# Kernel optimization log

Measured on AMD Instinct MI355X. Metric: run time of the kernel, lower is better.

## Reference

```python
import jax, jax.numpy as jnp
import numpy as np

B = 32; D = 512; NH = 8; DH = 64; DEPTH = 8; MLP = 2048
NC = 256; Hs = 16; Ws = 16; SHIFT = 1
INNER = NH * DH


def setup_inputs() -> dict:
    key = jax.random.key(0)
    ks = jax.random.split(key, 8)
    s = D ** -0.5
    return {
        "z": jax.random.normal(ks[0], (B, D, Hs, Ws), jnp.float32),
        "slots": jax.random.normal(ks[1], (B, NC, D), jnp.float32),
        "pos_emb": jax.random.normal(ks[2], (1, Hs * Ws, D), jnp.float32) * s,
        "slot_pos_emb": jax.random.normal(ks[3], (1, NC, D), jnp.float32) * s,
        "norm_w": jnp.ones((D,), jnp.float32),
        "norm_b": jnp.zeros((D,), jnp.float32),
        "ln1_w": jnp.ones((DEPTH, D), jnp.float32),
        "ln1_b": jnp.zeros((DEPTH, D), jnp.float32),
        "qkv_w": jax.random.normal(ks[4], (DEPTH, D, 3 * INNER), jnp.float32) * 0.02,
        "out_w": jax.random.normal(ks[5], (DEPTH, INNER, D), jnp.float32) * 0.02,
        "out_b": jnp.zeros((DEPTH, D), jnp.float32),
        "ln2_w": jnp.ones((DEPTH, D), jnp.float32),
        "ln2_b": jnp.zeros((DEPTH, D), jnp.float32),
        "mlp_w1": jax.random.normal(ks[6], (DEPTH, D, MLP), jnp.float32) * 0.02,
        "mlp_b1": jnp.zeros((DEPTH, MLP), jnp.float32),
        "mlp_w2": jax.random.normal(ks[7], (DEPTH, MLP, D), jnp.float32) * 0.02,
        "mlp_b2": jnp.zeros((DEPTH, D), jnp.float32),
    }


def _ln(x, w, b):
    m = x.mean(-1, keepdims=True)
    v = ((x - m) ** 2).mean(-1, keepdims=True)
    return (x - m) * jax.lax.rsqrt(v + 1e-5) * w + b


def reference(z, slots, pos_emb, slot_pos_emb, norm_w, norm_b,
              ln1_w, ln1_b, qkv_w, out_w, out_b,
              ln2_w, ln2_b, mlp_w1, mlp_b1, mlp_w2, mlp_b2):
    S = NC + Hs * Ws  # 512 tokens: carriers then patches
    mem = slots + slot_pos_emb                                   # [B, NC, D]
    h = z.reshape(B, D, Hs * Ws).transpose(0, 2, 1) + pos_emb    # [B, HW, D]
    x = jnp.concatenate([mem, h], axis=1)                        # [B, S, D]
    x = _ln(x, norm_w, norm_b)
    causal = jnp.tril(jnp.ones((S, S), dtype=bool))              # allowed positions
    scale = DH ** -0.5
    for i in range(DEPTH):
        y = _ln(x, ln1_w[i], ln1_b[i])
        qkv = y @ qkv_w[i]                                       # [B, S, 3*INNER]
        q, k, v = jnp.split(qkv, 3, axis=-1)
        q = q.reshape(B, S, NH, DH).transpose(0, 2, 1, 3)
        k = k.reshape(B, S, NH, DH).transpose(0, 2, 1, 3)
        v = v.reshape(B, S, NH, DH).transpose(0, 2, 1, 3)
        att = jnp.einsum('bhqd,bhkd->bhqk', q, k) * scale
        att = jnp.where(causal, att, jnp.float32(-1e30))
        att = jax.nn.softmax(att, axis=-1)
        o = jnp.einsum('bhqk,bhkd->bhqd', att, v)
        o = o.transpose(0, 2, 1, 3).reshape(B, S, INNER)
        x = x + o @ out_w[i] + out_b[i]
        y = _ln(x, ln2_w[i], ln2_b[i])
        x = x + jax.nn.gelu(y @ mlp_w1[i] + mlp_b1[i], approximate=False) @ mlp_w2[i] + mlp_b2[i]
    out = x[:, NC - SHIFT:NC - SHIFT + Hs * Ws]                  # shifted slice
    return out.transpose(0, 2, 1).reshape(B, D, Hs, Ws)
```

## Files before the change

kernel.cpp:

```cpp
#include <hip/hip_runtime.h>
#include <hip/hip_bf16.h>
#include <math.h>

#define Bb 32
#define Dd 512
#define Ss 512
#define NHh 8
#define DHh 64
#define MLPm 2048
#define NCc 256
#define INNERi 512
#define Mrows (Bb*Ss)

typedef __bf16 bf16x8 __attribute__((ext_vector_type(8)));
typedef float floatx4 __attribute__((ext_vector_type(4)));

__device__ __forceinline__ void load_lds16(const void* g, void* l) {
  __builtin_amdgcn_global_load_lds(
      (__attribute__((address_space(1))) void*)(g),
      (__attribute__((address_space(3))) void*)(l), 16, 0, 0);
}

__device__ __forceinline__ int swz(int row, int seg) {
  return row * 64 + (((seg) ^ (row & 7)) << 3);
}

__global__ void transpose_w(const float* __restrict__ in, __hip_bfloat16* __restrict__ out,
                            int K, int N, size_t in_ls, size_t out_ls)
{
  __shared__ float tile[32][33];
  in  += (size_t)blockIdx.z * in_ls;
  out += (size_t)blockIdx.z * out_ls;
  int n0 = blockIdx.x * 32, k0 = blockIdx.y * 32;
  int tx = threadIdx.x;
  #pragma unroll
  for (int i = threadIdx.y; i < 32; i += 8)
    tile[i][tx] = in[(size_t)(k0 + i) * N + n0 + tx];
  __syncthreads();
  #pragma unroll
  for (int i = threadIdx.y; i < 32; i += 8)
    out[(size_t)(n0 + i) * K + k0 + tx] = __float2bfloat16(tile[tx][i]);
}

__global__ void prologue_kernel(const float* __restrict__ z, const float* __restrict__ slots,
                                const float* __restrict__ pos, const float* __restrict__ spos,
                                const float* __restrict__ nw, const float* __restrict__ nb,
                                float* __restrict__ x)
{
  int row = blockIdx.x;
  int b = row >> 9, s = row & 511;
  int lane = threadIdx.x;
  float v[8];
  float sum = 0.f;
  #pragma unroll
  for (int j = 0; j < 8; ++j) {
    int d = lane + j * 64;
    float t;
    if (s < NCc) t = slots[((size_t)b * NCc + s) * Dd + d] + spos[(size_t)s * Dd + d];
    else {
      int sp = s - NCc;
      t = z[((size_t)b * Dd + d) * 256 + sp] + pos[(size_t)sp * Dd + d];
    }
    v[j] = t; sum += t;
  }
  #pragma unroll
  for (int o = 32; o; o >>= 1) sum += __shfl_xor(sum, o);
  float mean = sum * (1.f / Dd);
  float vs = 0.f;
  #pragma unroll
  for (int j = 0; j < 8; ++j) { float d = v[j] - mean; vs += d * d; }
  #pragma unroll
  for (int o = 32; o; o >>= 1) vs += __shfl_xor(vs, o);
  float rs = rsqrtf(vs * (1.f / Dd) + 1e-5f);
  #pragma unroll
  for (int j = 0; j < 8; ++j) {
    int d = lane + j * 64;
    x[(size_t)row * Dd + d] = (v[j] - mean) * rs * nw[d] + nb[d];
  }
}

__global__ void ln_kernel(const float* __restrict__ x, const float* __restrict__ w,
                          const float* __restrict__ b, __hip_bfloat16* __restrict__ y)
{
  int row = blockIdx.x * 4 + (threadIdx.x >> 6);
  int lane = threadIdx.x & 63;
  const float* xr = x + (size_t)row * Dd;
  float v[8];
  float sum = 0.f;
  #pragma unroll
  for (int j = 0; j < 8; ++j) { v[j] = xr[lane + j * 64]; sum += v[j]; }
  #pragma unroll
  for (int o = 32; o; o >>= 1) sum += __shfl_xor(sum, o);
  float mean = sum * (1.f / Dd);
  float vs = 0.f;
  #pragma unroll
  for (int j = 0; j < 8; ++j) { float d = v[j] - mean; vs += d * d; }
  #pragma unroll
  for (int o = 32; o; o >>= 1) vs += __shfl_xor(vs, o);
  float rs = rsqrtf(vs * (1.f / Dd) + 1e-5f);
  #pragma unroll
  for (int j = 0; j < 8; ++j) {
    int d = lane + j * 64;
    y[(size_t)row * Dd + d] = __float2bfloat16((v[j] - mean) * rs * w[d] + b[d]);
  }
}

template <int MODE>
__global__ __launch_bounds__(256, 2)
void gemm_bt(const __hip_bfloat16* __restrict__ A, const __hip_bfloat16* __restrict__ Bt,
             const float* __restrict__ bias, const float* __restrict__ res,
             void* __restrict__ Out, int M, int N, int K)
{
  constexpr int BM = 128, BN = 128, BK = 64;
  __shared__ __align__(16) __hip_bfloat16 As[BM * BK];
  __shared__ __align__(16) __hip_bfloat16 Bs[BN * BK];
  const int tid = threadIdx.x;
  const int lane = tid & 63;
  const int wave = tid >> 6;

  const int NBLK = N >> 7;
  const int bid = blockIdx.x;
  const int xcd = bid & 7;
  const int j = bid >> 3;
  const int nb = j % NBLK;
  const int mt = xcd + ((j / NBLK) << 3);
  const int m0 = mt << 7;
  const int n0 = nb << 7;

  const int wm = (wave & 1) * 64;
  const int wn = (wave >> 1) * 64;
  const int quad = lane >> 4;
  const int lrow = lane & 15;

  floatx4 acc[4][4];
  #pragma unroll
  for (int i = 0; i < 4; ++i)
    #pragma unroll
    for (int jj = 0; jj < 4; ++jj) {
      floatx4 z4 = {0.f, 0.f, 0.f, 0.f};
      acc[i][jj] = z4;
    }

  for (int k0 = 0; k0 < K; k0 += BK) {
    #pragma unroll
    for (int it = 0; it < 4; ++it) {
      int c = it * 256 + tid;
      int row = c >> 3, seg = (c & 7) ^ (row & 7);
      load_lds16(A + (size_t)(m0 + row) * K + k0 + seg * 8, As + c * 8);
    }
    #pragma unroll
    for (int it = 0; it < 4; ++it) {
      int c = it * 256 + tid;
      int row = c >> 3, seg = (c & 7) ^ (row & 7);
      load_lds16(Bt + (size_t)(n0 + row) * K + k0 + seg * 8, Bs + c * 8);
    }
    __syncthreads();

    #pragma unroll
    for (int k1 = 0; k1 < BK; k1 += 32) {
      const int s0 = k1 >> 3;
      bf16x8 a[4], b[4];
      #pragma unroll
      for (int i = 0; i < 4; ++i)
        a[i] = *reinterpret_cast<const bf16x8*>(&As[swz(wm + i * 16 + lrow, s0 + quad)]);
      #pragma unroll
      for (int i = 0; i < 4; ++i)
        b[i] = *reinterpret_cast<const bf16x8*>(&Bs[swz(wn + i * 16 + lrow, s0 + quad)]);
      #pragma unroll
      for (int mi = 0; mi < 4; ++mi)
        #pragma unroll
        for (int ni = 0; ni < 4; ++ni)
          acc[mi][ni] = __builtin_amdgcn_mfma_f32_16x16x32_bf16(a[mi], b[ni], acc[mi][ni], 0, 0, 0);
    }
    __syncthreads();
  }

  #pragma unroll
  for (int mi = 0; mi < 4; ++mi) {
    #pragma unroll
    for (int r = 0; r < 4; ++r) {
      int gm = m0 + wm + mi * 16 + quad * 4 + r;
      #pragma unroll
      for (int ni = 0; ni < 4; ++ni) {
        int gn = n0 + wn + ni * 16 + lrow;
        float v = acc[mi][ni][r];
        size_t oi = (size_t)gm * N + gn;
        if (MODE == 0) {
          ((__hip_bfloat16*)Out)[oi] = __float2bfloat16(v);
        } else if (MODE == 1) {
          ((float*)Out)[oi] = v + bias[gn] + res[oi];
        } else {
          float t = v + bias[gn];
          float g = 0.5f * t * (1.0f + erff(t * 0.70710678118654752f));
          ((__hip_bfloat16*)Out)[oi] = __float2bfloat16(g);
        }
      }
    }
  }
}

#define GBAR()    asm volatile("s_barrier" ::: "memory")
#define GWAIT10() asm volatile("s_waitcnt vmcnt(10)" ::: "memory")
#define GWAIT0()  asm volatile("s_waitcnt vmcnt(0)" ::: "memory")
#define LGKM0()   do { asm volatile("s_waitcnt lgkmcnt(0)" ::: "memory"); \
                       __builtin_amdgcn_sched_barrier(0); } while (0)
#define DSR0(d,a)  asm volatile("ds_read_b128 %0, %1"             : "=v"(d) : "v"(a))
#define DSR1(d,a)  asm volatile("ds_read_b128 %0, %1 offset:1024" : "=v"(d) : "v"(a))
#define DSR2(d,a)  asm volatile("ds_read_b128 %0, %1 offset:2048" : "=v"(d) : "v"(a))
#define DSR3(d,a)  asm volatile("ds_read_b128 %0, %1 offset:3072" : "=v"(d) : "v"(a))

template <int MODE>
__global__ __launch_bounds__(512, 2)
void gemm256(const __hip_bfloat16* __restrict__ A, const __hip_bfloat16* __restrict__ Bt,
             const float* __restrict__ bias, void* __restrict__ Out,
             int M, int N, int K)
{
  extern __shared__ __hip_bfloat16 lds[];
  const int tid  = threadIdx.x;
  const int lane = tid & 63;
  const int wave = tid >> 6;
  const int wm = wave >> 2, wn = wave & 3;
  const int quad = lane >> 4, lrow = lane & 15;

  const int NBN = N >> 8;
  const int nwg = gridDim.x;
  const int bid = blockIdx.x;
  const int qq = nwg >> 3, rr = nwg & 7;
  const int xcd = bid & 7, oin = bid >> 3;
  const int wg = (xcd < rr ? xcd * (qq + 1) : rr * (qq + 1) + (xcd - rr) * qq) + oin;
  const int m0 = (wg / NBN) << 8;
  const int n0 = (wg % NBN) << 8;
  const int NT = K >> 6;

  const int srow = tid >> 2;
  const int sseg = (tid & 3) ^ ((tid >> 3) & 3);
  const __hip_bfloat16* gA = A  + (size_t)(m0 + srow) * K + sseg * 8;
  const __hip_bfloat16* gB = Bt + (size_t)(n0 + srow) * K + sseg * 8;
  const size_t gstep = (size_t)128 * K;

  __hip_bfloat16* const Abase = lds;
  __hip_bfloat16* const Bbase = lds + 32768;

  auto stageA = [&](int t, int kh) {
    int ts = t < NT ? t : NT - 1;
    int kb = ts * 64 + kh * 32;
    __hip_bfloat16* d = Abase + ((((t & 1) << 1) | kh) * 8192) + tid * 8;
    load_lds16(gA + kb, d);
    load_lds16(gA + gstep + kb, d + 4096);
  };
  auto stageB = [&](int t, int kh) {
    int ts = t < NT ? t : NT - 1;
    int kb = ts * 64 + kh * 32;
    __hip_bfloat16* d = Bbase + ((((t & 1) << 1) | kh) * 8192) + tid * 8;
    load_lds16(gB + kb, d);
    load_lds16(gB + gstep + kb, d + 4096);
  };

  floatx4 acc[2][4][4];
  #pragma unroll
  for (int mh = 0; mh < 2; ++mh)
    #pragma unroll
    for (int mi = 0; mi < 4; ++mi)
      #pragma unroll
      for (int ni = 0; ni < 4; ++ni) {
        floatx4 z4 = {0.f, 0.f, 0.f, 0.f};
        acc[mh][mi][ni] = z4;
      }

  const uint32_t ldsA = (uint32_t)(size_t)(__attribute__((address_space(3))) void*)Abase;
  const uint32_t ldsB = (uint32_t)(size_t)(__attribute__((address_space(3))) void*)Bbase;
  const uint32_t rsegb = (uint32_t)((quad ^ ((lrow >> 1) & 3)) << 4);
  const uint32_t arow_b = (uint32_t)((wm * 128 + lrow) * 64) + rsegb;
  const uint32_t brow_b = (uint32_t)((wn * 64 + lrow) * 64) + rsegb;

  stageB(0, 0); stageA(0, 0); stageB(0, 1); stageA(0, 1);
  stageB(1, 0); stageA(1, 0); stageB(1, 1);
  GWAIT10();
  GBAR();

  bf16x8 af[4], bfr[4];
  for (int t = 0; t < NT; ++t) {
    const uint32_t aS = ldsA + (uint32_t)((t & 1) * 32768);
    const uint32_t bS = ldsB + (uint32_t)((t & 1) * 32768);
    const uint32_t a0 = aS + arow_b;
    const uint32_t b0 = bS + brow_b;
    const uint32_t a1 = aS + 16384 + arow_b;
    const uint32_t b1 = bS + 16384 + brow_b;

    DSR0(bfr[0], b0); DSR1(bfr[1], b0); DSR2(bfr[2], b0); DSR3(bfr[3], b0);
    DSR0(af[0], a0);  DSR1(af[1], a0);  DSR2(af[2], a0);  DSR3(af[3], a0);
    stageA(t + 1, 1);
    GBAR();
    LGKM0();
    __builtin_amdgcn_s_setprio(1);
    #pragma unroll
    for (int mi = 0; mi < 4; ++mi)
      #pragma unroll
      for (int ni = 0; ni < 4; ++ni)
        acc[0][mi][ni] = __builtin_amdgcn_mfma_f32_16x16x32_bf16(af[mi], bfr[ni], acc[0][mi][ni], 0, 0, 0);
    __builtin_amdgcn_s_setprio(0);
    GBAR();

    DSR0(af[0], a0 + 4096); DSR1(af[1], a0 + 4096);
    DSR2(af[2], a0 + 4096); DSR3(af[3], a0 + 4096);
    stageB(t + 2, 0);
    GBAR();
    LGKM0();
    __builtin_amdgcn_s_setprio(1);
    #pragma unroll
    for (int mi = 0; mi < 4; ++mi)
      #pragma unroll
      for (int ni = 0; ni < 4; ++ni)
        acc[1][mi][ni] = __builtin_amdgcn_mfma_f32_16x16x32_bf16(af[mi], bfr[ni], acc[1][mi][ni], 0, 0, 0);
    __builtin_amdgcn_s_setprio(0);
    GWAIT10();
    GBAR();

    DSR0(bfr[0], b1); DSR1(bfr[1], b1); DSR2(bfr[2], b1); DSR3(bfr[3], b1);
    DSR0(af[0], a1);  DSR1(af[1], a1);  DSR2(af[2], a1);  DSR3(af[3], a1);
    stageA(t + 2, 0);
    GBAR();
    LGKM0();
    __builtin_amdgcn_s_setprio(1);
    #pragma unroll
    for (int mi = 0; mi < 4; ++mi)
      #pragma unroll
      for (int ni = 0; ni < 4; ++ni)
        acc[0][mi][ni] = __builtin_amdgcn_mfma_f32_16x16x32_bf16(af[mi], bfr[ni], acc[0][mi][ni], 0, 0, 0);
    __builtin_amdgcn_s_setprio(0);
    GBAR();

    DSR0(af[0], a1 + 4096); DSR1(af[1], a1 + 4096);
    DSR2(af[2], a1 + 4096); DSR3(af[3], a1 + 4096);
    stageB(t + 2, 1);
    GBAR();
    LGKM0();
    __builtin_amdgcn_s_setprio(1);
    #pragma unroll
    for (int mi = 0; mi < 4; ++mi)
      #pragma unroll
      for (int ni = 0; ni < 4; ++ni)
        acc[1][mi][ni] = __builtin_amdgcn_mfma_f32_16x16x32_bf16(af[mi], bfr[ni], acc[1][mi][ni], 0, 0, 0);
    __builtin_amdgcn_s_setprio(0);
    GWAIT10();
    GBAR();
  }

  GWAIT0();

  const int cm0 = m0 + wm * 128 + quad * 4;
  const int cn0 = n0 + wn * 64 + lrow;
  #pragma unroll
  for (int mh = 0; mh < 2; ++mh)
    #pragma unroll
    for (int mi = 0; mi < 4; ++mi)
      #pragma unroll
      for (int r = 0; r < 4; ++r) {
        const int gm = cm0 + mh * 64 + mi * 16 + r;
        #pragma unroll
        for (int ni = 0; ni < 4; ++ni) {
          const int gn = cn0 + ni * 16;
          float v = acc[mh][mi][ni][r];
          size_t oi = (size_t)gm * N + gn;
          if (MODE == 0) {
            ((__hip_bfloat16*)Out)[oi] = __float2bfloat16(v);
          } else {
            float tt = v + bias[gn];
            float g = 0.5f * tt * (1.0f + erff(tt * 0.70710678118654752f));
            ((__hip_bfloat16*)Out)[oi] = __float2bfloat16(g);
          }
        }
      }
}

__global__ __launch_bounds__(256, 2)
void attn_pair(const __hip_bfloat16* __restrict__ qkv, __hip_bfloat16* __restrict__ o)
{
  const int p = blockIdx.x;
  const int h = blockIdx.y, b = blockIdx.z;
  const int t0 = p, t1 = 7 - p;

  __shared__ __align__(16) __hip_bfloat16 Qs[2][64 * 64];
  __shared__ __align__(16) __hip_bfloat16 Ks[64 * 64];
  __shared__ __align__(16) __hip_bfloat16 Vt[64 * 64];
  __shared__ __align__(16) __hip_bfloat16 Ps[4][16 * 64];

  const int tid = threadIdx.x, lane = tid & 63, wave = tid >> 6;
  const int quad = lane >> 4, col = lane & 15;
  const size_t base = ((size_t)b * Ss) * 1536 + (size_t)h * 64;

  #pragma unroll
  for (int t = 0; t < 2; ++t) {
    const int tq = t ? t1 : t0;
    #pragma unroll
    for (int it = 0; it < 2; ++it) {
      int c = it * 256 + tid;
      int row = c >> 3, seg = c & 7;
      bf16x8 q8 = *reinterpret_cast<const bf16x8*>(
          qkv + base + (size_t)(tq * 64 + row) * 1536 + seg * 8);
      *reinterpret_cast<bf16x8*>(&Qs[t][swz(row, seg)]) = q8;
    }
  }

  bf16x8 kreg[2], vreg[2];
  auto load_kv = [&](int c0) {
    #pragma unroll
    for (int it = 0; it < 2; ++it) {
      int c = it * 256 + tid;
      kreg[it] = *reinterpret_cast<const bf16x8*>(
          qkv + base + 512 + (size_t)(c0 * 64 + (c >> 3)) * 1536 + (c & 7) * 8);
    }
    #pragma unroll
    for (int it = 0; it < 2; ++it) {
      int row = tid & 63, seg = it * 4 + wave;
      vreg[it] = *reinterpret_cast<const bf16x8*>(
          qkv + base + 1024 + (size_t)(c0 * 64 + row) * 1536 + seg * 8);
    }
  };
  auto store_kv = [&]() {
    #pragma unroll
    for (int it = 0; it < 2; ++it) {
      int c = it * 256 + tid;
      *reinterpret_cast<bf16x8*>(&Ks[swz(c >> 3, c & 7)]) = kreg[it];
    }
    #pragma unroll
    for (int it = 0; it < 2; ++it) {
      int row = tid & 63, seg = it * 4 + wave;
      union { bf16x8 v; __hip_bfloat16 e[8]; } u; u.v = vreg[it];
      #pragma unroll
      for (int j = 0; j < 8; ++j) {
        int d = seg * 8 + j;
        Vt[d * 64 + ((((row >> 3)) ^ (d & 7)) << 3) + (row & 7)] = u.e[j];
      }
    }
  };

  float  mrow[2][4], lsum[2][4];
  floatx4 accO[2][4];
  #pragma unroll
  for (int t = 0; t < 2; ++t)
    #pragma unroll
    for (int r = 0; r < 4; ++r) {
      mrow[t][r] = -1e30f; lsum[t][r] = 0.f;
      floatx4 z4 = {0.f, 0.f, 0.f, 0.f};
      accO[t][r] = z4;
    }

  auto compute_tile = [&](const __hip_bfloat16* Qt, int tq, int c,
                          float* mr, float* ls, floatx4* aO) {
    floatx4 accS[4];
    #pragma unroll
    for (int i = 0; i < 4; ++i) { floatx4 z4 = {0.f,0.f,0.f,0.f}; accS[i] = z4; }
    const int m = wave * 16 + col;
    #pragma unroll
    for (int kc = 0; kc < 2; ++kc) {
      bf16x8 aq = *reinterpret_cast<const bf16x8*>(&Qt[swz(m, kc * 4 + quad)]);
      #pragma unroll
      for (int ni = 0; ni < 4; ++ni) {
        bf16x8 bk = *reinterpret_cast<const bf16x8*>(&Ks[swz(ni * 16 + col, kc * 4 + quad)]);
        accS[ni] = __builtin_amdgcn_mfma_f32_16x16x32_bf16(aq, bk, accS[ni], 0, 0, 0);
      }
    }

    const bool diag = (c == tq);
    float sc[4][4];
    #pragma unroll
    for (int ni = 0; ni < 4; ++ni)
      #pragma unroll
      for (int r = 0; r < 4; ++r) {
        float s = accS[ni][r] * 0.125f;
        if (diag && (ni * 16 + col) > (wave * 16 + quad * 4 + r)) s = -1e30f;
        sc[ni][r] = s;
      }

    #pragma unroll
    for (int r = 0; r < 4; ++r) {
      float cm = fmaxf(fmaxf(sc[0][r], sc[1][r]), fmaxf(sc[2][r], sc[3][r]));
      #pragma unroll
      for (int off = 1; off < 16; off <<= 1) cm = fmaxf(cm, __shfl_xor(cm, off));
      float mnew = fmaxf(mr[r], cm);
      float alpha = __expf(mr[r] - mnew);
      mr[r] = mnew;
      float ps = 0.f;
      #pragma unroll
      for (int ni = 0; ni < 4; ++ni) {
        float pv = __expf(sc[ni][r] - mnew);
        sc[ni][r] = pv;
        ps += pv;
      }
      #pragma unroll
      for (int off = 1; off < 16; off <<= 1) ps += __shfl_xor(ps, off);
      ls[r] = ls[r] * alpha + ps;
      #pragma unroll
      for (int ni = 0; ni < 4; ++ni) aO[ni][r] *= alpha;
    }

    #pragma unroll
    for (int ni = 0; ni < 4; ++ni)
      #pragma unroll
      for (int r = 0; r < 4; ++r) {
        int prow = quad * 4 + r;
        int pseg = ni * 2 + (col >> 3);
        Ps[wave][prow * 64 + ((pseg ^ (prow & 7)) << 3) + (col & 7)] =
            __float2bfloat16(sc[ni][r]);
      }

    #pragma unroll
    for (int kc = 0; kc < 2; ++kc) {
      bf16x8 ap = *reinterpret_cast<const bf16x8*>(&Ps[wave][swz(col, kc * 4 + quad)]);
      #pragma unroll
      for (int ni = 0; ni < 4; ++ni) {
        bf16x8 bv = *reinterpret_cast<const bf16x8*>(&Vt[swz(ni * 16 + col, kc * 4 + quad)]);
        aO[ni] = __builtin_amdgcn_mfma_f32_16x16x32_bf16(ap, bv, aO[ni], 0, 0, 0);
      }
    }
  };

  load_kv(0);
  for (int c = 0; c <= t1; ++c) {
    __syncthreads();
    store_kv();
    __syncthreads();
    if (c < t1) load_kv(c + 1);
    compute_tile(Qs[1], t1, c, mrow[1], lsum[1], accO[1]);
    if (c <= t0) compute_tile(Qs[0], t0, c, mrow[0], lsum[0], accO[0]);
  }

  #pragma unroll
  for (int t = 0; t < 2; ++t) {
    const int tq = t ? t1 : t0;
    float inv[4];
    #pragma unroll
    for (int r = 0; r < 4; ++r) inv[r] = 1.f / lsum[t][r];
    #pragma unroll
    for (int ni = 0; ni < 4; ++ni)
      #pragma unroll
      for (int r = 0; r < 4; ++r) {
        int qg = tq * 64 + wave * 16 + quad * 4 + r;
        o[((size_t)b * Ss + qg) * INNERi + h * 64 + ni * 16 + col] =
            __float2bfloat16(accO[t][ni][r] * inv[r]);
      }
  }
}

__global__ void epilogue_kernel(const float* __restrict__ x, float* __restrict__ out)
{
  int idx = blockIdx.x * 256 + threadIdx.x;
  int sp = idx & 255;
  int bd = idx >> 8;
  int b = bd >> 9, d = bd & 511;
  out[idx] = x[((size_t)b * Ss + (NCc - 1) + sp) * Dd + d];
}

extern "C" void kernel_launch(void* const* d_in, const int* in_sizes, int n_in,
                              void* d_out, int out_size, void* d_ws, size_t ws_size,
                              hipStream_t stream)
{
  const float* z       = (const float*)d_in[0];
  const float* slots   = (const float*)d_in[1];
  const float* pos_emb = (const float*)d_in[2];
  const float* spos    = (const float*)d_in[3];
  const float* norm_w  = (const float*)d_in[4];
  const float* norm_b  = (const float*)d_in[5];
  const float* ln1_w   = (const float*)d_in[6];
  const float* ln1_b   = (const float*)d_in[7];
  const float* qkv_w   = (const float*)d_in[8];
  const float* out_w   = (const float*)d_in[9];
  const float* out_b   = (const float*)d_in[10];
  const float* ln2_w   = (const float*)d_in[11];
  const float* ln2_b   = (const float*)d_in[12];
  const float* mlp_w1  = (const float*)d_in[13];
  const float* mlp_b1  = (const float*)d_in[14];
  const float* mlp_w2  = (const float*)d_in[15];
  const float* mlp_b2  = (const float*)d_in[16];

  char* ws = (char*)d_ws;
  float*          xbuf = (float*)ws;
  __hip_bfloat16* ybuf = (__hip_bfloat16*)(ws + 33554432);
  __hip_bfloat16* qkvb = (__hip_bfloat16*)(ws + 50331648);
  __hip_bfloat16* obuf = (__hip_bfloat16*)(ws + 100663296);
  __hip_bfloat16* hbuf = (__hip_bfloat16*)(ws + 50331648);
  __hip_bfloat16* wT   = (__hip_bfloat16*)(ws + 117440512);

  const size_t WL = 3145728;

  hipFuncSetAttribute(reinterpret_cast<const void*>(&gemm256<0>),
                      hipFuncAttributeMaxDynamicSharedMemorySize, 131072);
  hipFuncSetAttribute(reinterpret_cast<const void*>(&gemm256<2>),
                      hipFuncAttributeMaxDynamicSharedMemorySize, 131072);

  dim3 tb(32, 8);
  transpose_w<<<dim3(1536 / 32, 512 / 32, 8), tb, 0, stream>>>(qkv_w,  wT + 0,       512, 1536, (size_t)512 * 1536, WL);
  transpose_w<<<dim3(512 / 32,  512 / 32, 8), tb, 0, stream>>>(out_w,  wT + 786432,  512, 512,  (size_t)512 * 512,  WL);
  transpose_w<<<dim3(2048 / 32, 512 / 32, 8), tb, 0, stream>>>(mlp_w1, wT + 1048576, 512, 2048, (size_t)512 * 2048, WL);
  transpose_w<<<dim3(512 / 32, 2048 / 32, 8), tb, 0, stream>>>(mlp_w2, wT + 2097152, 2048, 512, (size_t)2048 * 512, WL);

  prologue_kernel<<<Mrows, 64, 0, stream>>>(z, slots, pos_emb, spos, norm_w, norm_b, xbuf);

  for (int i = 0; i < 8; ++i) {
    const __hip_bfloat16* qkvT = wT + (size_t)i * WL;
    const __hip_bfloat16* outT = wT + (size_t)i * WL + 786432;
    const __hip_bfloat16* w1T  = wT + (size_t)i * WL + 1048576;
    const __hip_bfloat16* w2T  = wT + (size_t)i * WL + 2097152;

    ln_kernel<<<Mrows / 4, 256, 0, stream>>>(xbuf, ln1_w + i * Dd, ln1_b + i * Dd, ybuf);
    gemm256<0><<<dim3((1536 / 256) * (Mrows / 256)), 512, 131072, stream>>>(
        ybuf, qkvT, nullptr, qkvb, Mrows, 1536, 512);
    attn_pair<<<dim3(4, NHh, Bb), 256, 0, stream>>>(qkvb, obuf);
    gemm_bt<1><<<dim3((512 / 128) * (Mrows / 128)), 256, 0, stream>>>(
        obuf, outT, out_b + i * Dd, xbuf, xbuf, Mrows, 512, 512);
    ln_kernel<<<Mrows / 4, 256, 0, stream>>>(xbuf, ln2_w + i * Dd, ln2_b + i * Dd, ybuf);
    gemm256<2><<<dim3((2048 / 256) * (Mrows / 256)), 512, 131072, stream>>>(
        ybuf, w1T, mlp_b1 + i * MLPm, hbuf, Mrows, 2048, 512);
    gemm_bt<1><<<dim3((512 / 128) * (Mrows / 128)), 256, 0, stream>>>(
        hbuf, w2T, mlp_b2 + i * Dd, xbuf, xbuf, Mrows, 512, 2048);
  }

  epilogue_kernel<<<(Bb * Dd * 256) / 256, 256, 0, stream>>>(xbuf, (float*)d_out);
}
```

Baseline: 1.960 ms.

## Restructure GEMM main loop into two phases with full-K-tile fragment loads

Each 256x256 GEMM K-tile iteration now runs in two compute phases instead of four. A and B are staged as full 64-wide K tiles, and each phase reads both 32-wide K halves of the fragments and issues 32 MFMAs. This halves the number of barriers and LDS-wait points per tile and changes the wait count to vmcnt(4). The trade-offs are double-size fragment registers and a shorter window for global prefetches to hide before they are consumed.

```diff
diff --git a/kernel.cpp b/kernel.cpp
--- a/kernel.cpp
+++ b/kernel.cpp
@@ -200,14 +200,12 @@
 }
 
 #define GBAR()    asm volatile("s_barrier" ::: "memory")
-#define GWAIT10() asm volatile("s_waitcnt vmcnt(10)" ::: "memory")
+#define GWAIT4()  asm volatile("s_waitcnt vmcnt(4)" ::: "memory")
 #define GWAIT0()  asm volatile("s_waitcnt vmcnt(0)" ::: "memory")
 #define LGKM0()   do { asm volatile("s_waitcnt lgkmcnt(0)" ::: "memory"); \
                        __builtin_amdgcn_sched_barrier(0); } while (0)
-#define DSR0(d,a)  asm volatile("ds_read_b128 %0, %1"             : "=v"(d) : "v"(a))
-#define DSR1(d,a)  asm volatile("ds_read_b128 %0, %1 offset:1024" : "=v"(d) : "v"(a))
-#define DSR2(d,a)  asm volatile("ds_read_b128 %0, %1 offset:2048" : "=v"(d) : "v"(a))
-#define DSR3(d,a)  asm volatile("ds_read_b128 %0, %1 offset:3072" : "=v"(d) : "v"(a))
+#define DSRO(d,a,OFFSTR) asm volatile("ds_read_b128 %0, %1 offset:" OFFSTR \
+                                      : "=v"(d) : "v"(a))
 
 template <int MODE>
 __global__ __launch_bounds__(512, 2)
@@ -241,19 +239,23 @@
   __hip_bfloat16* const Abase = lds;
   __hip_bfloat16* const Bbase = lds + 32768;
 
-  auto stageA = [&](int t, int kh) {
+  auto stageApair = [&](int t) {
     int ts = t < NT ? t : NT - 1;
-    int kb = ts * 64 + kh * 32;
-    __hip_bfloat16* d = Abase + ((((t & 1) << 1) | kh) * 8192) + tid * 8;
+    int kb = ts * 64;
+    __hip_bfloat16* d = Abase + ((t & 1) * 2) * 8192 + tid * 8;
     load_lds16(gA + kb, d);
     load_lds16(gA + gstep + kb, d + 4096);
+    load_lds16(gA + kb + 32, d + 8192);
+    load_lds16(gA + gstep + kb + 32, d + 12288);
   };
-  auto stageB = [&](int t, int kh) {
+  auto stageBpair = [&](int t) {
     int ts = t < NT ? t : NT - 1;
-    int kb = ts * 64 + kh * 32;
-    __hip_bfloat16* d = Bbase + ((((t & 1) << 1) | kh) * 8192) + tid * 8;
+    int kb = ts * 64;
+    __hip_bfloat16* d = Bbase + ((t & 1) * 2) * 8192 + tid * 8;
     load_lds16(gB + kb, d);
     load_lds16(gB + gstep + kb, d + 4096);
+    load_lds16(gB + kb + 32, d + 8192);
+    load_lds16(gB + gstep + kb + 32, d + 12288);
   };
 
   floatx4 acc[2][4][4];
@@ -273,76 +275,54 @@
   const uint32_t arow_b = (uint32_t)((wm * 128 + lrow) * 64) + rsegb;
   const uint32_t brow_b = (uint32_t)((wn * 64 + lrow) * 64) + rsegb;
 
-  stageB(0, 0); stageA(0, 0); stageB(0, 1); stageA(0, 1);
-  stageB(1, 0); stageA(1, 0); stageB(1, 1);
-  GWAIT10();
+  stageBpair(0); stageApair(0); stageBpair(1);
+  GWAIT4();
   GBAR();
 
-  bf16x8 af[4], bfr[4];
+  bf16x8 af[2][4], bfr[2][4];
   for (int t = 0; t < NT; ++t) {
-    const uint32_t aS = ldsA + (uint32_t)((t & 1) * 32768);
-    const uint32_t bS = ldsB + (uint32_t)((t & 1) * 32768);
-    const uint32_t a0 = aS + arow_b;
-    const uint32_t b0 = bS + brow_b;
-    const uint32_t a1 = aS + 16384 + arow_b;
-    const uint32_t b1 = bS + 16384 + brow_b;
-
-    DSR0(bfr[0], b0); DSR1(bfr[1], b0); DSR2(bfr[2], b0); DSR3(bfr[3], b0);
-    DSR0(af[0], a0);  DSR1(af[1], a0);  DSR2(af[2], a0);  DSR3(af[3], a0);
-    stageA(t + 1, 1);
+    const uint32_t aA = ldsA + (uint32_t)((t & 1) * 32768) + arow_b;
+    const uint32_t bA = ldsB + (uint32_t)((t & 1) * 32768) + brow_b;
+
+    stageApair(t + 1);
+    DSRO(bfr[0][0], bA, "0");     DSRO(bfr[0][1], bA, "1024");
+    DSRO(bfr[0][2], bA, "2048");  DSRO(bfr[0][3], bA, "3072");
+    DSRO(bfr[1][0], bA, "16384"); DSRO(bfr[1][1], bA, "17408");
+    DSRO(bfr[1][2], bA, "18432"); DSRO(bfr[1][3], bA, "19456");
+    DSRO(af[0][0], aA, "0");      DSRO(af[0][1], aA, "1024");
+    DSRO(af[0][2], aA, "2048");   DSRO(af[0][3], aA, "3072");
+    DSRO(af[1][0], aA, "16384");  DSRO(af[1][1], aA, "17408");
+    DSRO(af[1][2], aA, "18432");  DSRO(af[1][3], aA, "19456");
     GBAR();
     LGKM0();
     __builtin_amdgcn_s_setprio(1);
     #pragma unroll
-    for (int mi = 0; mi < 4; ++mi)
-      #pragma unroll
-      for (int ni = 0; ni < 4; ++ni)
-        acc[0][mi][ni] = __builtin_amdgcn_mfma_f32_16x16x32_bf16(af[mi], bfr[ni], acc[0][mi][ni], 0, 0, 0);
+    for (int ks = 0; ks < 2; ++ks)
+      #pragma unroll
+      for (int mi = 0; mi < 4; ++mi)
+        #pragma unroll
+        for (int ni = 0; ni < 4; ++ni)
+          acc[0][mi][ni] = __builtin_amdgcn_mfma_f32_16x16x32_bf16(af[ks][mi], bfr[ks][ni], acc[0][mi][ni], 0, 0, 0);
     __builtin_amdgcn_s_setprio(0);
     GBAR();
 
-    DSR0(af[0], a0 + 4096); DSR1(af[1], a0 + 4096);
-    DSR2(af[2], a0 + 4096); DSR3(af[3], a0 + 4096);
-    stageB(t + 2, 0);
+    stageBpair(t + 2);
+    DSRO(af[0][0], aA, "4096");   DSRO(af[0][1], aA, "5120");
+    DSRO(af[0][2], aA, "6144");   DSRO(af[0][3], aA, "7168");
+    DSRO(af[1][0], aA, "20480");  DSRO(af[1][1], aA, "21504");
+    DSRO(af[1][2], aA, "22528");  DSRO(af[1][3], aA, "23552");
     GBAR();
     LGKM0();
     __builtin_amdgcn_s_setprio(1);
     #pragma unroll
-    for (int mi = 0; mi < 4; ++mi)
-      #pragma unroll
-      for (int ni = 0; ni < 4; ++ni)
-        acc[1][mi][ni] = __builtin_amdgcn_mfma_f32_16x16x32_bf16(af[mi], bfr[ni], acc[1][mi][ni], 0, 0, 0);
+    for (int ks = 0; ks < 2; ++ks)
+      #pragma unroll
+      for (int mi = 0; mi < 4; ++mi)
+        #pragma unroll
+        for (int ni = 0; ni < 4; ++ni)
+          acc[1][mi][ni] = __builtin_amdgcn_mfma_f32_16x16x32_bf16(af[ks][mi], bfr[ks][ni], acc[1][mi][ni], 0, 0, 0);
     __builtin_amdgcn_s_setprio(0);
-    GWAIT10();
-    GBAR();
-
-    DSR0(bfr[0], b1); DSR1(bfr[1], b1); DSR2(bfr[2], b1); DSR3(bfr[3], b1);
-    DSR0(af[0], a1);  DSR1(af[1], a1);  DSR2(af[2], a1);  DSR3(af[3], a1);
-    stageA(t + 2, 0);
-    GBAR();
-    LGKM0();
-    __builtin_amdgcn_s_setprio(1);
-    #pragma unroll
-    for (int mi = 0; mi < 4; ++mi)
-      #pragma unroll
-      for (int ni = 0; ni < 4; ++ni)
-        acc[0][mi][ni] = __builtin_amdgcn_mfma_f32_16x16x32_bf16(af[mi], bfr[ni], acc[0][mi][ni], 0, 0, 0);
-    __builtin_amdgcn_s_setprio(0);
-    GBAR();
-
-    DSR0(af[0], a1 + 4096); DSR1(af[1], a1 + 4096);
-    DSR2(af[2], a1 + 4096); DSR3(af[3], a1 + 4096);
-    stageB(t + 2, 1);
-    GBAR();
-    LGKM0();
-    __builtin_amdgcn_s_setprio(1);
-    #pragma unroll
-    for (int mi = 0; mi < 4; ++mi)
-      #pragma unroll
-      for (int ni = 0; ni < 4; ++ni)
-        acc[1][mi][ni] = __builtin_amdgcn_mfma_f32_16x16x32_bf16(af[mi], bfr[ni], acc[1][mi][ni], 0, 0, 0);
-    __builtin_amdgcn_s_setprio(0);
-    GWAIT10();
+    GWAIT4();
     GBAR();
   }
 
```

After: 2.112 ms. 7.7% more time.
